# Optimization experiments

Hardware: AMD Instinct MI355X
Metric: run time of the kernel (lower is better)

The kernel has to match this reference:

```python
import jax, jax.numpy as jnp
import numpy as np

N, E, H = 100000, 640000, 64
DIN_N, DIN_E, L, OUT = 32, 16, 2, 1
BN_EPS = 1e-5


def setup_inputs() -> dict:
    key = jax.random.key(0)
    ks = iter(jax.random.split(key, 40))
    def p(shape, s=0.05):
        return jax.random.normal(next(ks), shape, dtype=jnp.float32) * s
    return {
        "x": jax.random.normal(next(ks), (N, DIN_N), dtype=jnp.float32),
        "edge_attr": jax.random.normal(next(ks), (E, DIN_E), dtype=jnp.float32),
        "src": jax.random.randint(next(ks), (E,), 0, N),
        "dst": jax.random.randint(next(ks), (E,), 0, N),
        "node_emb_w": p((DIN_N, H)), "node_emb_b": p((H,)),
        "edge_emb_w": p((DIN_E, H)), "edge_emb_b": p((H,)),
        "lin_edge_w": p((L, H, H)), "lin_edge_b": p((L, H)),
        "conv_w1": p((L, H, H)), "conv_b1": p((L, H)),
        "conv_w2": p((L, H, H)), "conv_b2": p((L, H)),
        "emlp_w1": p((L, 3 * H, H)), "emlp_b1": p((L, H)),
        "emlp_w2": p((L, H, H)), "emlp_b2": p((L, H)),
        "bn_gamma": jnp.ones((L, H), jnp.float32),
        "bn_beta": jnp.zeros((L, H), jnp.float32),
        "mlp_w1": p((3 * H, 50)), "mlp_b1": p((50,)),
        "mlp_w2": p((50, 25)), "mlp_b2": p((25,)),
        "mlp_w3": p((25, OUT)), "mlp_b3": p((OUT,)),
    }


def _batchnorm(h, gamma, beta):
    # training-mode BatchNorm1d over the node axis (biased variance)
    mu = jnp.mean(h, axis=0)
    var = jnp.mean(jnp.square(h - mu), axis=0)
    return gamma * (h - mu) * jax.lax.rsqrt(var + BN_EPS) + beta


def _forward(x, edge_attr, src, dst,
             node_emb_w, node_emb_b, edge_emb_w, edge_emb_b,
             lin_edge_w, lin_edge_b, conv_w1, conv_b1, conv_w2, conv_b2,
             emlp_w1, emlp_b1, emlp_w2, emlp_b2, bn_gamma, bn_beta,
             mlp_w1, mlp_b1, mlp_w2, mlp_b2, mlp_w3, mlp_b3):
    x = x @ node_emb_w + node_emb_b                       # [N, H]
    e = edge_attr @ edge_emb_w + edge_emb_b               # [E, H]
    for i in range(L):
        # GINEConv (eps=0): msg = ReLU(x_src + Lin(edge_attr)); sum at dst
        msg = jax.nn.relu(x[src] + e @ lin_edge_w[i] + lin_edge_b[i])
        agg = jax.ops.segment_sum(msg, dst, num_segments=N)
        h = x + agg
        h = jax.nn.relu(h @ conv_w1[i] + conv_b1[i]) @ conv_w2[i] + conv_b2[i]
        x = (x + jax.nn.relu(_batchnorm(h, bn_gamma[i], bn_beta[i]))) / 2
        cat = jnp.concatenate([x[src], x[dst], e], axis=-1)  # [E, 3H]
        upd = jax.nn.relu(cat @ emlp_w1[i] + emlp_b1[i]) @ emlp_w2[i] + emlp_b2[i]
        e = e + upd / 2
    # edge readout: relu(cat(x_src, x_dst)) ++ edge_attr -> MLP (dropout off/eval)
    er = jnp.concatenate(
        [jax.nn.relu(jnp.concatenate([x[src], x[dst]], axis=-1)), e], axis=-1)
    hmid = jax.nn.relu(er @ mlp_w1 + mlp_b1)
    hmid = jax.nn.relu(hmid @ mlp_w2 + mlp_b2)
    logit = hmid @ mlp_w3 + mlp_b3
    return x, logit


def reference(x, edge_attr, src, dst,
              node_emb_w, node_emb_b, edge_emb_w, edge_emb_b,
              lin_edge_w, lin_edge_b, conv_w1, conv_b1, conv_w2, conv_b2,
              emlp_w1, emlp_b1, emlp_w2, emlp_b2, bn_gamma, bn_beta,
              mlp_w1, mlp_b1, mlp_w2, mlp_b2, mlp_w3, mlp_b3):
    return _forward(x, edge_attr, src, dst,
                    node_emb_w, node_emb_b, edge_emb_w, edge_emb_b,
                    lin_edge_w, lin_edge_b, conv_w1, conv_b1, conv_w2, conv_b2,
                    emlp_w1, emlp_b1, emlp_w2, emlp_b2, bn_gamma, bn_beta,
                    mlp_w1, mlp_b1, mlp_w2, mlp_b2, mlp_w3, mlp_b3)
```

## Files before the change

kernel.cpp:

```cpp
#include <hip/hip_runtime.h>

#define NN 100000
#define NE 640000
#define NB_SCAN 98

typedef __attribute__((ext_vector_type(8))) short short8;
typedef __attribute__((ext_vector_type(4))) float f32x4;
typedef __attribute__((ext_vector_type(4))) ushort ushort4v;

__device__ __forceinline__ float bf2f(ushort u) {
    unsigned v = ((unsigned)u) << 16;
    return __builtin_bit_cast(float, v);
}
__device__ __forceinline__ ushort f2bf(float f) {
    unsigned u = __builtin_bit_cast(unsigned, f);
    u += 0x7fffu + ((u >> 16) & 1u);
    return (ushort)(u >> 16);
}
__device__ __forceinline__ short8 brelu(short8 v) {
    #pragma unroll
    for (int i = 0; i < 8; ++i) v[i] = (v[i] < (short)0) ? (short)0 : v[i];
    return v;
}

__global__ void k_hist(const int* __restrict__ dst, int* __restrict__ hist)
{
    int i = blockIdx.x * 256 + threadIdx.x;
    atomicAdd(&hist[dst[i]], 1);
}

__global__ __launch_bounds__(256) void k_scan_part(const int* __restrict__ hist,
                                                   int* __restrict__ rp,
                                                   int* __restrict__ parts)
{
    __shared__ int s[256];
    int b = blockIdx.x, t = threadIdx.x;
    int base = b * 1024 + t * 4;
    int v[4]; int sum = 0;
    #pragma unroll
    for (int i = 0; i < 4; ++i) { int idx = base + i; v[i] = (idx < NN) ? hist[idx] : 0; sum += v[i]; }
    s[t] = sum; __syncthreads();
    for (int off = 1; off < 256; off <<= 1) {
        int x = (t >= off) ? s[t - off] : 0;
        __syncthreads(); s[t] += x; __syncthreads();
    }
    int excl = s[t] - sum;
    if (t == 255) parts[b] = s[255];
    int run = excl;
    #pragma unroll
    for (int i = 0; i < 4; ++i) { int idx = base + i; if (idx < NN) rp[idx] = run; run += v[i]; }
}

__global__ void k_scan_tops(int* __restrict__ parts, int* __restrict__ rp)
{
    __shared__ int s[128];
    int t = threadIdx.x;
    int v = (t < NB_SCAN) ? parts[t] : 0;
    s[t] = v; __syncthreads();
    for (int off = 1; off < 128; off <<= 1) {
        int x = (t >= off) ? s[t - off] : 0;
        __syncthreads(); s[t] += x; __syncthreads();
    }
    parts[t] = s[t] - v;
    if (t == 0) rp[NN] = NE;
}

__global__ __launch_bounds__(256) void k_scan_add(int* __restrict__ rp,
                                                  const int* __restrict__ parts,
                                                  int* __restrict__ cursor)
{
    int i = blockIdx.x * 256 + threadIdx.x;
    if (i >= NN) return;
    int v = rp[i] + parts[i >> 10];
    rp[i] = v; cursor[i] = v;
}

__global__ void k_scatter(const int* __restrict__ src, const int* __restrict__ dst,
                          int* __restrict__ cursor, int* __restrict__ eidx,
                          int* __restrict__ ssrc)
{
    int i = blockIdx.x * 256 + threadIdx.x;
    int d = dst[i];
    int p = atomicAdd(&cursor[d], 1);
    eidx[p] = i; ssrc[p] = src[i];
}

__global__ void k_w_subtile(const float* __restrict__ w, ushort* __restrict__ out,
                            int K, int Nin)
{
    int t = blockIdx.x * 256 + threadIdx.x;
    if (t >= K * 64) return;
    int k = t >> 6, c = t & 63;
    float v = (c < Nin) ? w[k * Nin + c] : 0.f;
    out[((k >> 3) * 64 + c) * 8 + (k & 7)] = f2bf(v);
}

__global__ void k_w_padk(const float* __restrict__ w, ushort* __restrict__ out,
                         int Kreal, int Kpad)
{
    int t = blockIdx.x * 256 + threadIdx.x;
    if (t >= Kpad * 64) return;
    int k = t >> 6, c = t & 63;
    float v = (k < Kreal) ? w[k * 64 + c] : 0.f;
    out[((k >> 3) * 64 + c) * 8 + (k & 7)] = f2bf(v);
}

__global__ void k_w_msg(const float* __restrict__ lw, ushort* __restrict__ out)
{
    int t = blockIdx.x * 256 + threadIdx.x;
    if (t >= 128 * 64) return;
    int k = t >> 6, c = t & 63;
    float v = (k < 64) ? (k == c ? 1.f : 0.f) : lw[(k - 64) * 64 + c];
    out[((k >> 3) * 64 + c) * 8 + (k & 7)] = f2bf(v);
}

__global__ __launch_bounds__(256) void k_node_emb_mfma(
    const float* __restrict__ xin, const ushort* __restrict__ ws,
    const float* __restrict__ b, float* __restrict__ xout,
    ushort* __restrict__ xb)
{
    __shared__ ushort wl[32 * 64];
    __shared__ float fbuf[4][16 * 64];
    __shared__ ushort bbuf[4][16 * 64];
    int tid = threadIdx.x;
    *(short8*)&wl[tid * 8] = *(const short8*)&ws[tid * 8];
    __syncthreads();

    int wid = tid >> 6, lane = tid & 63, c = lane & 15, kg = lane >> 4;
    int t = blockIdx.x * 4 + wid;
    if (t >= NN / 16) return;
    int n0 = t * 16;

    const float* xr = xin + (size_t)(n0 + c) * 32 + kg * 8;
    f32x4 u0 = *(const f32x4*)xr, u1 = *(const f32x4*)(xr + 4);
    short8 a;
    #pragma unroll
    for (int j = 0; j < 4; ++j) { a[j] = (short)f2bf(u0[j]); a[4 + j] = (short)f2bf(u1[j]); }

    f32x4 acc[4];
    #pragma unroll
    for (int nt = 0; nt < 4; ++nt) {
        float bv = b[nt * 16 + c];
        acc[nt] = f32x4{bv, bv, bv, bv};
        short8 bf = *(const short8*)&wl[(kg * 64 + nt * 16 + c) * 8];
        acc[nt] = __builtin_amdgcn_mfma_f32_16x16x32_bf16(a, bf, acc[nt], 0, 0, 0);
    }
    #pragma unroll
    for (int nt = 0; nt < 4; ++nt)
        #pragma unroll
        for (int i = 0; i < 4; ++i) {
            int rr = kg * 4 + i, cc = nt * 16 + c;
            float v = acc[nt][i];
            fbuf[wid][rr * 64 + cc] = v;
            bbuf[wid][rr * 64 + cc] = f2bf(v);
        }
    #pragma unroll
    for (int r = 0; r < 4; ++r) {
        int q = r * 64 + lane;
        *(f32x4*)&xout[(size_t)(n0 + (q >> 4)) * 64 + (q & 15) * 4] =
            *(f32x4*)&fbuf[wid][q * 4];
    }
    #pragma unroll
    for (int r = 0; r < 2; ++r) {
        int q = r * 64 + lane;
        *(short8*)&xb[(size_t)(n0 + (q >> 3)) * 64 + (q & 7) * 8] =
            *(short8*)&bbuf[wid][q * 8];
    }
}

__global__ __launch_bounds__(256) void k_edge_emb_mfma(
    const float* __restrict__ ein, const ushort* __restrict__ ws,
    const float* __restrict__ b, ushort* __restrict__ eb)
{
    __shared__ ushort wl[32 * 64];
    __shared__ ushort bbuf[4][16 * 64];
    int tid = threadIdx.x;
    *(short8*)&wl[tid * 8] = *(const short8*)&ws[tid * 8];
    __syncthreads();

    int wid = tid >> 6, lane = tid & 63, c = lane & 15, kg = lane >> 4;
    int t = blockIdx.x * 4 + wid;
    int e0 = t * 16;

    short8 a = (short8)0;
    if (kg < 2) {
        const float* er = ein + (size_t)(e0 + c) * 16 + kg * 8;
        f32x4 u0 = *(const f32x4*)er, u1 = *(const f32x4*)(er + 4);
        #pragma unroll
        for (int j = 0; j < 4; ++j) { a[j] = (short)f2bf(u0[j]); a[4 + j] = (short)f2bf(u1[j]); }
    }
    f32x4 acc[4];
    #pragma unroll
    for (int nt = 0; nt < 4; ++nt) {
        float bv = b[nt * 16 + c];
        acc[nt] = f32x4{bv, bv, bv, bv};
        short8 bf = *(const short8*)&wl[(kg * 64 + nt * 16 + c) * 8];
        acc[nt] = __builtin_amdgcn_mfma_f32_16x16x32_bf16(a, bf, acc[nt], 0, 0, 0);
    }
    #pragma unroll
    for (int nt = 0; nt < 4; ++nt)
        #pragma unroll
        for (int i = 0; i < 4; ++i)
            bbuf[wid][(kg * 4 + i) * 64 + nt * 16 + c] = f2bf(acc[nt][i]);
    #pragma unroll
    for (int r = 0; r < 2; ++r) {
        int q = r * 64 + lane;
        *(short8*)&eb[(size_t)(e0 + (q >> 3)) * 64 + (q & 7) * 8] =
            *(short8*)&bbuf[wid][q * 8];
    }
}

__global__ __launch_bounds__(256) void k_msgA(
    const ushort* __restrict__ xb, const ushort* __restrict__ eb,
    const int* __restrict__ eidx, const int* __restrict__ ssrc,
    const ushort* __restrict__ wms, const float* __restrict__ lb,
    ushort* __restrict__ msgbuf)
{
    __shared__ ushort wl[128 * 64];
    __shared__ ushort bbuf[4][16 * 64];
    int tid = threadIdx.x;
    #pragma unroll
    for (int i = 0; i < 4; ++i)
        *(short8*)&wl[(i * 256 + tid) * 8] = *(const short8*)&wms[(i * 256 + tid) * 8];
    __syncthreads();

    int wid = tid >> 6, lane = tid & 63;
    int c = lane & 15, kg = lane >> 4;
    float bv[4];
    #pragma unroll
    for (int nt = 0; nt < 4; ++nt) bv[nt] = lb[nt * 16 + c];

    #pragma unroll 1
    for (int t4 = 0; t4 < 4; ++t4) {
        int p0 = blockIdx.x * 256 + wid * 64 + t4 * 16;
        int row = p0 + c;
        int edge = eidx[row], s = ssrc[row];
        const ushort* xs = xb + (size_t)s * 64;
        const ushort* ee = eb + (size_t)edge * 64;
        short8 a[4];
        a[0] = *(const short8*)(xs + kg * 8);
        a[1] = *(const short8*)(xs + 32 + kg * 8);
        a[2] = *(const short8*)(ee + kg * 8);
        a[3] = *(const short8*)(ee + 32 + kg * 8);

        f32x4 acc[4];
        #pragma unroll
        for (int nt = 0; nt < 4; ++nt) acc[nt] = f32x4{bv[nt], bv[nt], bv[nt], bv[nt]};
        #pragma unroll
        for (int ks = 0; ks < 4; ++ks) {
            #pragma unroll
            for (int nt = 0; nt < 4; ++nt) {
                short8 bf = *(const short8*)&wl[((ks * 4 + kg) * 64 + nt * 16 + c) * 8];
                acc[nt] = __builtin_amdgcn_mfma_f32_16x16x32_bf16(a[ks], bf, acc[nt], 0, 0, 0);
            }
        }
        #pragma unroll
        for (int nt = 0; nt < 4; ++nt)
            #pragma unroll
            for (int i = 0; i < 4; ++i)
                bbuf[wid][(kg * 4 + i) * 64 + nt * 16 + c] = f2bf(fmaxf(acc[nt][i], 0.f));
        #pragma unroll
        for (int r = 0; r < 2; ++r) {
            int q = r * 64 + lane;
            *(short8*)&msgbuf[(size_t)(p0 + (q >> 3)) * 64 + (q & 7) * 8] =
                *(short8*)&bbuf[wid][q * 8];
        }
    }
}

__global__ __launch_bounds__(256) void k_conv_csr(
    const float* __restrict__ x, const ushort* __restrict__ msgbuf,
    const int* __restrict__ rp, float* __restrict__ hout,
    const ushort* __restrict__ w1s, const float* __restrict__ b1,
    const ushort* __restrict__ w2s, const float* __restrict__ b2,
    float* __restrict__ stats)
{
    __shared__ ushort w1l[64 * 64];
    __shared__ ushort w2l[64 * 64];
    __shared__ ushort h1l[4][1024];
    __shared__ float red[2][4][64];
    int tid = threadIdx.x;
    #pragma unroll
    for (int i = 0; i < 2; ++i) {
        *(short8*)&w1l[(i * 256 + tid) * 8] = *(const short8*)&w1s[(i * 256 + tid) * 8];
        *(short8*)&w2l[(i * 256 + tid) * 8] = *(const short8*)&w2s[(i * 256 + tid) * 8];
    }
    __syncthreads();

    int wid = tid >> 6, lane = tid & 63;
    int c = lane & 15, kg = lane >> 4;

    short8 w2f[2][4];
    #pragma unroll
    for (int ks = 0; ks < 2; ++ks)
        #pragma unroll
        for (int nt = 0; nt < 4; ++nt)
            w2f[ks][nt] = *(const short8*)&w2l[((ks * 4 + kg) * 64 + nt * 16 + c) * 8];

    float b1v[4], b2v[4];
    #pragma unroll
    for (int nt = 0; nt < 4; ++nt) { b1v[nt] = b1[nt * 16 + c]; b2v[nt] = b2[nt * 16 + c]; }

    float s1[4] = {0.f, 0.f, 0.f, 0.f}, s2[4] = {0.f, 0.f, 0.f, 0.f};
    ushort* hl = h1l[wid];

    int t = blockIdx.x * 4 + wid;
    if (t < NN / 16) {
        int n0 = t * 16;
        int n = n0 + c;
        int jb = rp[n], je = rp[n + 1];
        float sm0[8] = {0,0,0,0,0,0,0,0}, sm1[8] = {0,0,0,0,0,0,0,0};
        for (int j = jb; j < je; ++j) {
            short8 m0 = *(const short8*)&msgbuf[(size_t)j * 64 + kg * 8];
            short8 m1 = *(const short8*)&msgbuf[(size_t)j * 64 + 32 + kg * 8];
            #pragma unroll
            for (int i = 0; i < 8; ++i) {
                sm0[i] += bf2f((ushort)m0[i]);
                sm1[i] += bf2f((ushort)m1[i]);
            }
        }
        const float* xr = x + (size_t)n * 64;
        f32x4 u0 = *(const f32x4*)(xr + kg * 8);
        f32x4 u1 = *(const f32x4*)(xr + kg * 8 + 4);
        f32x4 v0 = *(const f32x4*)(xr + 32 + kg * 8);
        f32x4 v1 = *(const f32x4*)(xr + 32 + kg * 8 + 4);
        short8 a[2];
        #pragma unroll
        for (int j = 0; j < 4; ++j) {
            a[0][j]     = (short)f2bf(u0[j] + sm0[j]);
            a[0][4 + j] = (short)f2bf(u1[j] + sm0[4 + j]);
            a[1][j]     = (short)f2bf(v0[j] + sm1[j]);
            a[1][4 + j] = (short)f2bf(v1[j] + sm1[4 + j]);
        }
        f32x4 acc[4];
        #pragma unroll
        for (int nt = 0; nt < 4; ++nt) acc[nt] = f32x4{b1v[nt], b1v[nt], b1v[nt], b1v[nt]};
        #pragma unroll
        for (int ks = 0; ks < 2; ++ks) {
            #pragma unroll
            for (int nt = 0; nt < 4; ++nt) {
                short8 bf = *(const short8*)&w1l[((ks * 4 + kg) * 64 + nt * 16 + c) * 8];
                acc[nt] = __builtin_amdgcn_mfma_f32_16x16x32_bf16(a[ks], bf, acc[nt], 0, 0, 0);
            }
        }
        #pragma unroll
        for (int nt = 0; nt < 4; ++nt) {
            #pragma unroll
            for (int i = 0; i < 4; ++i) {
                int rr = kg * 4 + i, cc = nt * 16 + c;
                hl[((cc >> 3) * 16 + rr) * 8 + (cc & 7)] = f2bf(fmaxf(acc[nt][i], 0.f));
            }
        }
        f32x4 acc2[4];
        #pragma unroll
        for (int nt = 0; nt < 4; ++nt) acc2[nt] = f32x4{b2v[nt], b2v[nt], b2v[nt], b2v[nt]};
        #pragma unroll
        for (int ks = 0; ks < 2; ++ks) {
            short8 ha = *(const short8*)&hl[((ks * 4 + kg) * 16 + c) * 8];
            #pragma unroll
            for (int nt = 0; nt < 4; ++nt)
                acc2[nt] = __builtin_amdgcn_mfma_f32_16x16x32_bf16(ha, w2f[ks][nt], acc2[nt], 0, 0, 0);
        }
        #pragma unroll
        for (int nt = 0; nt < 4; ++nt) {
            #pragma unroll
            for (int i = 0; i < 4; ++i) {
                int rr = kg * 4 + i, cc = nt * 16 + c;
                float h2 = acc2[nt][i];
                hout[(size_t)(n0 + rr) * 64 + cc] = h2;
                s1[nt] += h2;
                s2[nt] += h2 * h2;
            }
        }
    }
    #pragma unroll
    for (int nt = 0; nt < 4; ++nt) {
        float v1 = s1[nt], v2 = s2[nt];
        v1 += __shfl_xor(v1, 16); v1 += __shfl_xor(v1, 32);
        v2 += __shfl_xor(v2, 16); v2 += __shfl_xor(v2, 32);
        s1[nt] = v1; s2[nt] = v2;
    }
    if (lane < 16) {
        #pragma unroll
        for (int nt = 0; nt < 4; ++nt) {
            red[0][wid][nt * 16 + c] = s1[nt];
            red[1][wid][nt * 16 + c] = s2[nt];
        }
    }
    __syncthreads();
    if (wid == 0) {
        float a = red[0][0][lane] + red[0][1][lane] + red[0][2][lane] + red[0][3][lane];
        float b = red[1][0][lane] + red[1][1][lane] + red[1][2][lane] + red[1][3][lane];
        unsafeAtomicAdd(&stats[lane], a);
        unsafeAtomicAdd(&stats[64 + lane], b);
    }
}

__global__ void k_bnfin(float* __restrict__ stats,
                        const float* __restrict__ gamma,
                        const float* __restrict__ beta)
{
    int j = threadIdx.x;
    float mu = stats[j] * (1.f / NN);
    float var = stats[64 + j] * (1.f / NN) - mu * mu;
    float a = gamma[j] * rsqrtf(var + 1e-5f);
    stats[128 + j] = a;
    stats[192 + j] = beta[j] - mu * a;
}

__global__ __launch_bounds__(256) void k_xupd4(float* __restrict__ x,
                                               const float* __restrict__ h,
                                               const float* __restrict__ stats,
                                               ushort* __restrict__ xb)
{
    int idx = blockIdx.x * 256 + threadIdx.x;
    int j4 = (idx & 15) * 4;
    f32x4 hv = *(const f32x4*)&h[(size_t)idx * 4];
    f32x4 xv = *(const f32x4*)&x[(size_t)idx * 4];
    f32x4 av = *(const f32x4*)&stats[128 + j4];
    f32x4 cv = *(const f32x4*)&stats[192 + j4];
    f32x4 xo;
    ushort4v bo;
    #pragma unroll
    for (int i = 0; i < 4; ++i) {
        float r = fmaxf(fmaf(hv[i], av[i], cv[i]), 0.f);
        float xn = (xv[i] + r) * 0.5f;
        xo[i] = xn;
        bo[i] = f2bf(xn);
    }
    *(f32x4*)&x[(size_t)idx * 4] = xo;
    *(ushort4v*)&xb[(size_t)idx * 4] = bo;
}

__global__ __launch_bounds__(256) void k_emlp_mfma(
    const ushort* __restrict__ xb, ushort* __restrict__ eb,
    const int* __restrict__ src, const int* __restrict__ dst,
    const ushort* __restrict__ w1s, const float* __restrict__ b1,
    const ushort* __restrict__ w2s, const float* __restrict__ b2)
{
    __shared__ ushort w1l[192 * 64];
    __shared__ ushort w2l[64 * 64];
    __shared__ ushort h1l[4][1024];
    int tid = threadIdx.x;
    #pragma unroll
    for (int i = 0; i < 6; ++i)
        *(short8*)&w1l[(i * 256 + tid) * 8] = *(const short8*)&w1s[(i * 256 + tid) * 8];
    #pragma unroll
    for (int i = 0; i < 2; ++i)
        *(short8*)&w2l[(i * 256 + tid) * 8] = *(const short8*)&w2s[(i * 256 + tid) * 8];
    __syncthreads();

    int wid = tid >> 6, lane = tid & 63;
    int c = lane & 15, kg = lane >> 4;

    short8 w2f[2][4];
    #pragma unroll
    for (int ks = 0; ks < 2; ++ks)
        #pragma unroll
        for (int nt = 0; nt < 4; ++nt)
            w2f[ks][nt] = *(const short8*)&w2l[((ks * 4 + kg) * 64 + nt * 16 + c) * 8];

    float b1v[4], b2v[4];
    #pragma unroll
    for (int nt = 0; nt < 4; ++nt) { b1v[nt] = b1[nt * 16 + c]; b2v[nt] = b2[nt * 16 + c]; }

    ushort* hl = h1l[wid];

    #pragma unroll 1
    for (int t4 = 0; t4 < 4; ++t4) {
        int e0 = blockIdx.x * 256 + wid * 64 + t4 * 16;
        int myedge = e0 + c;
        int s = src[myedge], d = dst[myedge];
        const ushort* xs = xb + (size_t)s * 64;
        const ushort* xd = xb + (size_t)d * 64;
        const ushort* ee = eb + (size_t)myedge * 64;
        short8 a[6];
        a[0] = *(const short8*)(xs + kg * 8);
        a[1] = *(const short8*)(xs + 32 + kg * 8);
        a[2] = *(const short8*)(xd + kg * 8);
        a[3] = *(const short8*)(xd + 32 + kg * 8);
        a[4] = *(const short8*)(ee + kg * 8);
        a[5] = *(const short8*)(ee + 32 + kg * 8);

        f32x4 acc[4];
        #pragma unroll
        for (int nt = 0; nt < 4; ++nt) acc[nt] = f32x4{b1v[nt], b1v[nt], b1v[nt], b1v[nt]};
        #pragma unroll
        for (int ks = 0; ks < 6; ++ks) {
            #pragma unroll
            for (int nt = 0; nt < 4; ++nt) {
                short8 bf = *(const short8*)&w1l[((ks * 4 + kg) * 64 + nt * 16 + c) * 8];
                acc[nt] = __builtin_amdgcn_mfma_f32_16x16x32_bf16(a[ks], bf, acc[nt], 0, 0, 0);
            }
        }
        #pragma unroll
        for (int nt = 0; nt < 4; ++nt) {
            #pragma unroll
            for (int i = 0; i < 4; ++i) {
                int rr = kg * 4 + i, cc = nt * 16 + c;
                hl[((cc >> 3) * 16 + rr) * 8 + (cc & 7)] = f2bf(fmaxf(acc[nt][i], 0.f));
            }
        }
        f32x4 acc2[4];
        #pragma unroll
        for (int nt = 0; nt < 4; ++nt) acc2[nt] = f32x4{b2v[nt], b2v[nt], b2v[nt], b2v[nt]};
        #pragma unroll
        for (int ks = 0; ks < 2; ++ks) {
            short8 ha = *(const short8*)&hl[((ks * 4 + kg) * 16 + c) * 8];
            #pragma unroll
            for (int nt = 0; nt < 4; ++nt)
                acc2[nt] = __builtin_amdgcn_mfma_f32_16x16x32_bf16(ha, w2f[ks][nt], acc2[nt], 0, 0, 0);
        }
        #pragma unroll
        for (int nt = 0; nt < 4; ++nt) {
            #pragma unroll
            for (int i = 0; i < 4; ++i) {
                int rr = kg * 4 + i, cc = nt * 16 + c;
                size_t off = (size_t)(e0 + rr) * 64 + cc;
                eb[off] = f2bf(bf2f(eb[off]) + 0.5f * acc2[nt][i]);
            }
        }
    }
}

__global__ __launch_bounds__(256) void k_readout_mfma(
    const ushort* __restrict__ xb, const ushort* __restrict__ eb,
    const int* __restrict__ src, const int* __restrict__ dst,
    const ushort* __restrict__ w1s, const float* __restrict__ b1,
    const float* __restrict__ w2, const float* __restrict__ b2,
    const float* __restrict__ w3, const float* __restrict__ b3,
    float* __restrict__ logit)
{
    __shared__ ushort w1l[192 * 64];
    __shared__ ushort hw[4][64 * 50];
    int tid = threadIdx.x;
    #pragma unroll
    for (int i = 0; i < 6; ++i)
        *(short8*)&w1l[(i * 256 + tid) * 8] = *(const short8*)&w1s[(i * 256 + tid) * 8];
    __syncthreads();

    int wid = tid >> 6, lane = tid & 63;
    int c = lane & 15, kg = lane >> 4;
    float b1v[4];
    #pragma unroll
    for (int nt = 0; nt < 4; ++nt) b1v[nt] = (nt * 16 + c < 50) ? b1[nt * 16 + c] : 0.f;

    #pragma unroll 1
    for (int t4 = 0; t4 < 4; ++t4) {
        int e0 = blockIdx.x * 256 + wid * 64 + t4 * 16;
        int myedge = e0 + c;
        int s = src[myedge], d = dst[myedge];
        const ushort* xs = xb + (size_t)s * 64;
        const ushort* xd = xb + (size_t)d * 64;
        const ushort* ee = eb + (size_t)myedge * 64;
        short8 a[6];
        a[0] = brelu(*(const short8*)(xs + kg * 8));
        a[1] = brelu(*(const short8*)(xs + 32 + kg * 8));
        a[2] = brelu(*(const short8*)(xd + kg * 8));
        a[3] = brelu(*(const short8*)(xd + 32 + kg * 8));
        a[4] = *(const short8*)(ee + kg * 8);
        a[5] = *(const short8*)(ee + 32 + kg * 8);

        f32x4 acc[4];
        #pragma unroll
        for (int nt = 0; nt < 4; ++nt) acc[nt] = f32x4{b1v[nt], b1v[nt], b1v[nt], b1v[nt]};
        #pragma unroll
        for (int ks = 0; ks < 6; ++ks) {
            #pragma unroll
            for (int nt = 0; nt < 4; ++nt) {
                short8 bf = *(const short8*)&w1l[((ks * 4 + kg) * 64 + nt * 16 + c) * 8];
                acc[nt] = __builtin_amdgcn_mfma_f32_16x16x32_bf16(a[ks], bf, acc[nt], 0, 0, 0);
            }
        }
        #pragma unroll
        for (int nt = 0; nt < 4; ++nt) {
            #pragma unroll
            for (int i = 0; i < 4; ++i) {
                int rr = kg * 4 + i, cc = nt * 16 + c;
                if (cc < 50)
                    hw[wid][(t4 * 16 + rr) * 50 + cc] = f2bf(fmaxf(acc[nt][i], 0.f));
            }
        }
    }
    int edge = blockIdx.x * 256 + wid * 64 + lane;
    const ushort* hrow = &hw[wid][lane * 50];
    float a25[25];
    #pragma unroll
    for (int j = 0; j < 25; ++j) a25[j] = b2[j];
    #pragma unroll 2
    for (int k = 0; k < 50; ++k) {
        float hv = bf2f(hrow[k]);
        #pragma unroll
        for (int j = 0; j < 25; ++j) a25[j] = fmaf(hv, w2[k * 25 + j], a25[j]);
    }
    float lg = b3[0];
    #pragma unroll
    for (int k = 0; k < 25; ++k) lg = fmaf(fmaxf(a25[k], 0.f), w3[k], lg);
    logit[edge] = lg;
}

extern "C" void kernel_launch(void* const* d_in, const int* in_sizes, int n_in,
                              void* d_out, int out_size, void* d_ws, size_t ws_size,
                              hipStream_t stream)
{
    const float* x_in  = (const float*)d_in[0];
    const float* eattr = (const float*)d_in[1];
    const int*   src   = (const int*)d_in[2];
    const int*   dst   = (const int*)d_in[3];
    const float* n_w   = (const float*)d_in[4];
    const float* n_b   = (const float*)d_in[5];
    const float* e_w   = (const float*)d_in[6];
    const float* e_b   = (const float*)d_in[7];
    const float* lw    = (const float*)d_in[8];
    const float* lb    = (const float*)d_in[9];
    const float* cw1   = (const float*)d_in[10];
    const float* cb1   = (const float*)d_in[11];
    const float* cw2   = (const float*)d_in[12];
    const float* cb2   = (const float*)d_in[13];
    const float* ew1   = (const float*)d_in[14];
    const float* eb1   = (const float*)d_in[15];
    const float* ew2   = (const float*)d_in[16];
    const float* eb2   = (const float*)d_in[17];
    const float* gam   = (const float*)d_in[18];
    const float* bet   = (const float*)d_in[19];
    const float* m1w   = (const float*)d_in[20];
    const float* m1b   = (const float*)d_in[21];
    const float* m2w   = (const float*)d_in[22];
    const float* m2b   = (const float*)d_in[23];
    const float* m3w   = (const float*)d_in[24];
    const float* m3b   = (const float*)d_in[25];

    float* xbuf  = (float*)d_out;
    float* logit = xbuf + (size_t)NN * 64;

    ushort* eb     = (ushort*)d_ws;
    float*  tmp    = (float*)(eb + (size_t)NE * 64);
    float*  stats  = tmp + (size_t)NN * 64;
    ushort* w1s    = (ushort*)(stats + 256);
    ushort* w2s    = w1s + 2 * 192 * 64;
    ushort* m1s    = w2s + 2 * 64 * 64;
    ushort* xb     = m1s + 192 * 64;
    ushort* wms    = xb + (size_t)NN * 64;
    ushort* cw1s   = wms + 2 * 128 * 64;
    ushort* cw2s   = cw1s + 2 * 64 * 64;
    ushort* nws    = cw2s + 2 * 64 * 64;
    ushort* ews    = nws + 32 * 64;
    ushort* msgbuf = ews + 32 * 64;
    int*    hist   = (int*)(msgbuf + (size_t)NE * 64);
    int*    rp     = hist + NN;
    int*    cursor = rp + NN + 1;
    int*    parts  = cursor + NN;
    int*    eidx   = parts + 128;
    int*    ssrc   = eidx + NE;

    hipMemsetAsync(hist, 0, NN * sizeof(int), stream);
    k_hist<<<NE / 256, 256, 0, stream>>>(dst, hist);
    k_scan_part<<<NB_SCAN, 256, 0, stream>>>(hist, rp, parts);
    k_scan_tops<<<1, 128, 0, stream>>>(parts, rp);
    k_scan_add<<<(NN + 255) / 256, 256, 0, stream>>>(rp, parts, cursor);
    k_scatter<<<NE / 256, 256, 0, stream>>>(src, dst, cursor, eidx, ssrc);

    k_w_subtile<<<48, 256, 0, stream>>>(ew1,            w1s,            192, 64);
    k_w_subtile<<<48, 256, 0, stream>>>(ew1 + 192 * 64, w1s + 192 * 64, 192, 64);
    k_w_subtile<<<16, 256, 0, stream>>>(ew2,            w2s,            64, 64);
    k_w_subtile<<<16, 256, 0, stream>>>(ew2 + 64 * 64,  w2s + 64 * 64,  64, 64);
    k_w_subtile<<<48, 256, 0, stream>>>(m1w,            m1s,            192, 50);
    k_w_msg<<<32, 256, 0, stream>>>(lw,           wms);
    k_w_msg<<<32, 256, 0, stream>>>(lw + 64 * 64, wms + 128 * 64);
    k_w_subtile<<<16, 256, 0, stream>>>(cw1,            cw1s,           64, 64);
    k_w_subtile<<<16, 256, 0, stream>>>(cw1 + 64 * 64,  cw1s + 64 * 64, 64, 64);
    k_w_subtile<<<16, 256, 0, stream>>>(cw2,            cw2s,           64, 64);
    k_w_subtile<<<16, 256, 0, stream>>>(cw2 + 64 * 64,  cw2s + 64 * 64, 64, 64);
    k_w_padk<<<8, 256, 0, stream>>>(n_w, nws, 32, 32);
    k_w_padk<<<8, 256, 0, stream>>>(e_w, ews, 16, 32);

    k_node_emb_mfma<<<(NN / 16 + 3) / 4, 256, 0, stream>>>(x_in, nws, n_b, xbuf, xb);
    k_edge_emb_mfma<<<NE / 64, 256, 0, stream>>>(eattr, ews, e_b, eb);

    for (int l = 0; l < 2; ++l) {
        hipMemsetAsync(stats, 0, 256 * sizeof(float), stream);
        k_msgA<<<NE / 256, 256, 0, stream>>>(xb, eb, eidx, ssrc,
                                             wms + l * 128 * 64, lb + l * 64, msgbuf);
        k_conv_csr<<<(NN / 16 + 3) / 4, 256, 0, stream>>>(
            xbuf, msgbuf, rp, tmp, cw1s + l * 64 * 64, cb1 + l * 64,
            cw2s + l * 64 * 64, cb2 + l * 64, stats);
        k_bnfin<<<1, 64, 0, stream>>>(stats, gam + l * 64, bet + l * 64);
        k_xupd4<<<NN * 16 / 256, 256, 0, stream>>>(xbuf, tmp, stats, xb);
        k_emlp_mfma<<<NE / 256, 256, 0, stream>>>(xb, eb, src, dst,
                                                  w1s + l * 192 * 64, eb1 + l * 64,
                                                  w2s + l * 64 * 64, eb2 + l * 64);
    }

    k_readout_mfma<<<NE / 256, 256, 0, stream>>>(xb, eb, src, dst,
                                                 m1s, m1b, m2w, m2b, m3w, m3b, logit);
}
```

Before: 578.2 us.

## Fuse GINE message computation into edge embedding and edge MLP kernels

```diff
diff --git a/kernel.cpp b/kernel.cpp
--- a/kernel.cpp
+++ b/kernel.cpp
@@ -75,14 +75,13 @@
     rp[i] = v; cursor[i] = v;
 }
 
-__global__ void k_scatter(const int* __restrict__ src, const int* __restrict__ dst,
-                          int* __restrict__ cursor, int* __restrict__ eidx,
-                          int* __restrict__ ssrc)
+__global__ void k_scatter(const int* __restrict__ dst,
+                          int* __restrict__ cursor, int* __restrict__ spos)
 {
     int i = blockIdx.x * 256 + threadIdx.x;
     int d = dst[i];
     int p = atomicAdd(&cursor[d], 1);
-    eidx[p] = i; ssrc[p] = src[i];
+    spos[i] = p;
 }
 
 __global__ void k_w_subtile(const float* __restrict__ w, ushort* __restrict__ out,
@@ -168,19 +167,26 @@
     }
 }
 
-__global__ __launch_bounds__(256) void k_edge_emb_mfma(
+__global__ __launch_bounds__(256) void k_edge_emb_fused(
     const float* __restrict__ ein, const ushort* __restrict__ ws,
-    const float* __restrict__ b, ushort* __restrict__ eb)
+    const float* __restrict__ b, ushort* __restrict__ eb,
+    const ushort* __restrict__ xb, const int* __restrict__ src,
+    const int* __restrict__ spos, const ushort* __restrict__ wm,
+    const float* __restrict__ lb, ushort* __restrict__ msgbuf)
 {
     __shared__ ushort wl[32 * 64];
-    __shared__ ushort bbuf[4][16 * 64];
+    __shared__ ushort wml[128 * 64];
+    __shared__ ushort bbuf[4][16 * 72];
     int tid = threadIdx.x;
     *(short8*)&wl[tid * 8] = *(const short8*)&ws[tid * 8];
+    #pragma unroll
+    for (int i = 0; i < 4; ++i)
+        *(short8*)&wml[(i * 256 + tid) * 8] = *(const short8*)&wm[(i * 256 + tid) * 8];
     __syncthreads();
 
     int wid = tid >> 6, lane = tid & 63, c = lane & 15, kg = lane >> 4;
-    int t = blockIdx.x * 4 + wid;
-    int e0 = t * 16;
+    int e0 = (blockIdx.x * 4 + wid) * 16;
+    ushort* bb = bbuf[wid];
 
     short8 a = (short8)0;
     if (kg < 2) {
@@ -201,71 +207,42 @@
     for (int nt = 0; nt < 4; ++nt)
         #pragma unroll
         for (int i = 0; i < 4; ++i)
-            bbuf[wid][(kg * 4 + i) * 64 + nt * 16 + c] = f2bf(acc[nt][i]);
+            bb[(kg * 4 + i) * 72 + nt * 16 + c] = f2bf(acc[nt][i]);
     #pragma unroll
     for (int r = 0; r < 2; ++r) {
         int q = r * 64 + lane;
         *(short8*)&eb[(size_t)(e0 + (q >> 3)) * 64 + (q & 7) * 8] =
-            *(short8*)&bbuf[wid][q * 8];
-    }
-}
-
-__global__ __launch_bounds__(256) void k_msgA(
-    const ushort* __restrict__ xb, const ushort* __restrict__ eb,
-    const int* __restrict__ eidx, const int* __restrict__ ssrc,
-    const ushort* __restrict__ wms, const float* __restrict__ lb,
-    ushort* __restrict__ msgbuf)
-{
-    __shared__ ushort wl[128 * 64];
-    __shared__ ushort bbuf[4][16 * 64];
-    int tid = threadIdx.x;
-    #pragma unroll
-    for (int i = 0; i < 4; ++i)
-        *(short8*)&wl[(i * 256 + tid) * 8] = *(const short8*)&wms[(i * 256 + tid) * 8];
-    __syncthreads();
-
-    int wid = tid >> 6, lane = tid & 63;
-    int c = lane & 15, kg = lane >> 4;
-    float bv[4];
-    #pragma unroll
-    for (int nt = 0; nt < 4; ++nt) bv[nt] = lb[nt * 16 + c];
-
-    #pragma unroll 1
-    for (int t4 = 0; t4 < 4; ++t4) {
-        int p0 = blockIdx.x * 256 + wid * 64 + t4 * 16;
-        int row = p0 + c;
-        int edge = eidx[row], s = ssrc[row];
-        const ushort* xs = xb + (size_t)s * 64;
-        const ushort* ee = eb + (size_t)edge * 64;
-        short8 a[4];
-        a[0] = *(const short8*)(xs + kg * 8);
-        a[1] = *(const short8*)(xs + 32 + kg * 8);
-        a[2] = *(const short8*)(ee + kg * 8);
-        a[3] = *(const short8*)(ee + 32 + kg * 8);
-
-        f32x4 acc[4];
-        #pragma unroll
-        for (int nt = 0; nt < 4; ++nt) acc[nt] = f32x4{bv[nt], bv[nt], bv[nt], bv[nt]};
-        #pragma unroll
-        for (int ks = 0; ks < 4; ++ks) {
-            #pragma unroll
-            for (int nt = 0; nt < 4; ++nt) {
-                short8 bf = *(const short8*)&wl[((ks * 4 + kg) * 64 + nt * 16 + c) * 8];
-                acc[nt] = __builtin_amdgcn_mfma_f32_16x16x32_bf16(a[ks], bf, acc[nt], 0, 0, 0);
-            }
-        }
-        #pragma unroll
-        for (int nt = 0; nt < 4; ++nt)
-            #pragma unroll
-            for (int i = 0; i < 4; ++i)
-                bbuf[wid][(kg * 4 + i) * 64 + nt * 16 + c] = f2bf(fmaxf(acc[nt][i], 0.f));
-        #pragma unroll
-        for (int r = 0; r < 2; ++r) {
-            int q = r * 64 + lane;
-            *(short8*)&msgbuf[(size_t)(p0 + (q >> 3)) * 64 + (q & 7) * 8] =
-                *(short8*)&bbuf[wid][q * 8];
-        }
-    }
+            *(short8*)&bb[(q >> 3) * 72 + (q & 7) * 8];
+    }
+    short8 en0 = *(const short8*)&bb[c * 72 + kg * 8];
+    short8 en1 = *(const short8*)&bb[c * 72 + 32 + kg * 8];
+    const ushort* xs = xb + (size_t)src[e0 + c] * 64;
+    short8 a0 = *(const short8*)(xs + kg * 8);
+    short8 a1 = *(const short8*)(xs + 32 + kg * 8);
+
+    f32x4 acc3[4];
+    #pragma unroll
+    for (int nt = 0; nt < 4; ++nt) {
+        float bv = lb[nt * 16 + c];
+        acc3[nt] = f32x4{bv, bv, bv, bv};
+    }
+    short8 af[4] = {a0, a1, en0, en1};
+    #pragma unroll
+    for (int ks = 0; ks < 4; ++ks) {
+        #pragma unroll
+        for (int nt = 0; nt < 4; ++nt) {
+            short8 bf = *(const short8*)&wml[((ks * 4 + kg) * 64 + nt * 16 + c) * 8];
+            acc3[nt] = __builtin_amdgcn_mfma_f32_16x16x32_bf16(af[ks], bf, acc3[nt], 0, 0, 0);
+        }
+    }
+    #pragma unroll
+    for (int nt = 0; nt < 4; ++nt)
+        #pragma unroll
+        for (int i = 0; i < 4; ++i)
+            bb[(kg * 4 + i) * 72 + nt * 16 + c] = f2bf(fmaxf(acc3[nt][i], 0.f));
+    int p = spos[e0 + c];
+    *(short8*)&msgbuf[(size_t)p * 64 + kg * 8]      = *(short8*)&bb[c * 72 + kg * 8];
+    *(short8*)&msgbuf[(size_t)p * 64 + 32 + kg * 8] = *(short8*)&bb[c * 72 + 32 + kg * 8];
 }
 
 __global__ __launch_bounds__(256) void k_conv_csr(
@@ -432,43 +409,46 @@
     *(ushort4v*)&xb[(size_t)idx * 4] = bo;
 }
 
-__global__ __launch_bounds__(256) void k_emlp_mfma(
+template<int NEXT>
+__global__ __launch_bounds__(512) void k_emlp_fused(
     const ushort* __restrict__ xb, ushort* __restrict__ eb,
     const int* __restrict__ src, const int* __restrict__ dst,
     const ushort* __restrict__ w1s, const float* __restrict__ b1,
-    const ushort* __restrict__ w2s, const float* __restrict__ b2)
+    const ushort* __restrict__ w2s, const float* __restrict__ b2,
+    const ushort* __restrict__ wm, const float* __restrict__ lbn,
+    const int* __restrict__ spos, ushort* __restrict__ msgbuf)
 {
     __shared__ ushort w1l[192 * 64];
     __shared__ ushort w2l[64 * 64];
-    __shared__ ushort h1l[4][1024];
+    __shared__ ushort wml[NEXT ? 128 * 64 : 8];
+    __shared__ ushort hb[8][1152];
     int tid = threadIdx.x;
     #pragma unroll
-    for (int i = 0; i < 6; ++i)
-        *(short8*)&w1l[(i * 256 + tid) * 8] = *(const short8*)&w1s[(i * 256 + tid) * 8];
-    #pragma unroll
-    for (int i = 0; i < 2; ++i)
-        *(short8*)&w2l[(i * 256 + tid) * 8] = *(const short8*)&w2s[(i * 256 + tid) * 8];
+    for (int i = 0; i < 3; ++i)
+        *(short8*)&w1l[(i * 512 + tid) * 8] = *(const short8*)&w1s[(i * 512 + tid) * 8];
+    *(short8*)&w2l[tid * 8] = *(const short8*)&w2s[tid * 8];
+    if (NEXT) {
+        #pragma unroll
+        for (int i = 0; i < 2; ++i)
+            *(short8*)&wml[(i * 512 + tid) * 8] = *(const short8*)&wm[(i * 512 + tid) * 8];
+    }
     __syncthreads();
 
     int wid = tid >> 6, lane = tid & 63;
     int c = lane & 15, kg = lane >> 4;
 
-    short8 w2f[2][4];
-    #pragma unroll
-    for (int ks = 0; ks < 2; ++ks)
-        #pragma unroll
-        for (int nt = 0; nt < 4; ++nt)
-            w2f[ks][nt] = *(const short8*)&w2l[((ks * 4 + kg) * 64 + nt * 16 + c) * 8];
-
-    float b1v[4], b2v[4];
-    #pragma unroll
-    for (int nt = 0; nt < 4; ++nt) { b1v[nt] = b1[nt * 16 + c]; b2v[nt] = b2[nt * 16 + c]; }
-
-    ushort* hl = h1l[wid];
+    float b1v[4], b2v[4], lbv[4];
+    #pragma unroll
+    for (int nt = 0; nt < 4; ++nt) {
+        b1v[nt] = b1[nt * 16 + c];
+        b2v[nt] = b2[nt * 16 + c];
+        lbv[nt] = NEXT ? lbn[nt * 16 + c] : 0.f;
+    }
+    ushort* hl = hb[wid];
 
     #pragma unroll 1
     for (int t4 = 0; t4 < 4; ++t4) {
-        int e0 = blockIdx.x * 256 + wid * 64 + t4 * 16;
+        int e0 = blockIdx.x * 512 + wid * 64 + t4 * 16;
         int myedge = e0 + c;
         int s = src[myedge], d = dst[myedge];
         const ushort* xs = xb + (size_t)s * 64;
@@ -508,17 +488,48 @@
         for (int ks = 0; ks < 2; ++ks) {
             short8 ha = *(const short8*)&hl[((ks * 4 + kg) * 16 + c) * 8];
             #pragma unroll
+            for (int nt = 0; nt < 4; ++nt) {
+                short8 bf = *(const short8*)&w2l[((ks * 4 + kg) * 64 + nt * 16 + c) * 8];
+                acc2[nt] = __builtin_amdgcn_mfma_f32_16x16x32_bf16(ha, bf, acc2[nt], 0, 0, 0);
+            }
+        }
+        #pragma unroll
+        for (int nt = 0; nt < 4; ++nt)
+            #pragma unroll
+            for (int i = 0; i < 4; ++i)
+                hl[(kg * 4 + i) * 72 + nt * 16 + c] = f2bf(acc2[nt][i]);
+        short8 u0 = *(const short8*)&hl[c * 72 + kg * 8];
+        short8 u1 = *(const short8*)&hl[c * 72 + 32 + kg * 8];
+        short8 en0, en1;
+        #pragma unroll
+        for (int j = 0; j < 8; ++j) {
+            en0[j] = (short)f2bf(bf2f((ushort)a[4][j]) + 0.5f * bf2f((ushort)u0[j]));
+            en1[j] = (short)f2bf(bf2f((ushort)a[5][j]) + 0.5f * bf2f((ushort)u1[j]));
+        }
+        *(short8*)&eb[(size_t)myedge * 64 + kg * 8]      = en0;
+        *(short8*)&eb[(size_t)myedge * 64 + 32 + kg * 8] = en1;
+
+        if (NEXT) {
+            f32x4 acc3[4];
+            #pragma unroll
+            for (int nt = 0; nt < 4; ++nt) acc3[nt] = f32x4{lbv[nt], lbv[nt], lbv[nt], lbv[nt]};
+            short8 af[4] = {a[0], a[1], en0, en1};
+            #pragma unroll
+            for (int ks = 0; ks < 4; ++ks) {
+                #pragma unroll
+                for (int nt = 0; nt < 4; ++nt) {
+                    short8 bf = *(const short8*)&wml[((ks * 4 + kg) * 64 + nt * 16 + c) * 8];
+                    acc3[nt] = __builtin_amdgcn_mfma_f32_16x16x32_bf16(af[ks], bf, acc3[nt], 0, 0, 0);
+                }
+            }
+            #pragma unroll
             for (int nt = 0; nt < 4; ++nt)
-                acc2[nt] = __builtin_amdgcn_mfma_f32_16x16x32_bf16(ha, w2f[ks][nt], acc2[nt], 0, 0, 0);
-        }
-        #pragma unroll
-        for (int nt = 0; nt < 4; ++nt) {
-            #pragma unroll
-            for (int i = 0; i < 4; ++i) {
-                int rr = kg * 4 + i, cc = nt * 16 + c;
-                size_t off = (size_t)(e0 + rr) * 64 + cc;
-                eb[off] = f2bf(bf2f(eb[off]) + 0.5f * acc2[nt][i]);
-            }
+                #pragma unroll
+                for (int i = 0; i < 4; ++i)
+                    hl[(kg * 4 + i) * 72 + nt * 16 + c] = f2bf(fmaxf(acc3[nt][i], 0.f));
+            int p = spos[myedge];
+            *(short8*)&msgbuf[(size_t)p * 64 + kg * 8]      = *(short8*)&hl[c * 72 + kg * 8];
+            *(short8*)&msgbuf[(size_t)p * 64 + 32 + kg * 8] = *(short8*)&hl[c * 72 + 32 + kg * 8];
         }
     }
 }
@@ -650,15 +661,14 @@
     int*    rp     = hist + NN;
     int*    cursor = rp + NN + 1;
     int*    parts  = cursor + NN;
-    int*    eidx   = parts + 128;
-    int*    ssrc   = eidx + NE;
+    int*    spos   = parts + 128;
 
     hipMemsetAsync(hist, 0, NN * sizeof(int), stream);
     k_hist<<<NE / 256, 256, 0, stream>>>(dst, hist);
     k_scan_part<<<NB_SCAN, 256, 0, stream>>>(hist, rp, parts);
     k_scan_tops<<<1, 128, 0, stream>>>(parts, rp);
     k_scan_add<<<(NN + 255) / 256, 256, 0, stream>>>(rp, parts, cursor);
-    k_scatter<<<NE / 256, 256, 0, stream>>>(src, dst, cursor, eidx, ssrc);
+    k_scatter<<<NE / 256, 256, 0, stream>>>(dst, cursor, spos);
 
     k_w_subtile<<<48, 256, 0, stream>>>(ew1,            w1s,            192, 64);
     k_w_subtile<<<48, 256, 0, stream>>>(ew1 + 192 * 64, w1s + 192 * 64, 192, 64);
@@ -675,20 +685,25 @@
     k_w_padk<<<8, 256, 0, stream>>>(e_w, ews, 16, 32);
 
     k_node_emb_mfma<<<(NN / 16 + 3) / 4, 256, 0, stream>>>(x_in, nws, n_b, xbuf, xb);
-    k_edge_emb_mfma<<<NE / 64, 256, 0, stream>>>(eattr, ews, e_b, eb);
+    k_edge_emb_fused<<<NE / 64, 256, 0, stream>>>(eattr, ews, e_b, eb,
+                                                  xb, src, spos, wms, lb, msgbuf);
 
     for (int l = 0; l < 2; ++l) {
         hipMemsetAsync(stats, 0, 256 * sizeof(float), stream);
-        k_msgA<<<NE / 256, 256, 0, stream>>>(xb, eb, eidx, ssrc,
-                                             wms + l * 128 * 64, lb + l * 64, msgbuf);
         k_conv_csr<<<(NN / 16 + 3) / 4, 256, 0, stream>>>(
             xbuf, msgbuf, rp, tmp, cw1s + l * 64 * 64, cb1 + l * 64,
             cw2s + l * 64 * 64, cb2 + l * 64, stats);
         k_bnfin<<<1, 64, 0, stream>>>(stats, gam + l * 64, bet + l * 64);
         k_xupd4<<<NN * 16 / 256, 256, 0, stream>>>(xbuf, tmp, stats, xb);
-        k_emlp_mfma<<<NE / 256, 256, 0, stream>>>(xb, eb, src, dst,
-                                                  w1s + l * 192 * 64, eb1 + l * 64,
-                                                  w2s + l * 64 * 64, eb2 + l * 64);
+        if (l == 0) {
+            k_emlp_fused<1><<<NE / 512, 512, 0, stream>>>(
+                xb, eb, src, dst, w1s, eb1, w2s, eb2,
+                wms + 128 * 64, lb + 64, spos, msgbuf);
+        } else {
+            k_emlp_fused<0><<<NE / 512, 512, 0, stream>>>(
+                xb, eb, src, dst, w1s + 192 * 64, eb1 + 64, w2s + 64 * 64, eb2 + 64,
+                wms, lb, spos, msgbuf);
+        }
     }
 
     k_readout_mfma<<<NE / 256, 256, 0, stream>>>(xb, eb, src, dst,
```

New measurement: 607.9 us. 1.05x slower.
